# Performance work log

Hardware: AMD Instinct MI355X
Metric: run time of the kernel (lower is better)

Reference implementation:

```python
import jax, jax.numpy as jnp
import numpy as np

D_MODEL = 1024
NHEAD = 16
DK = D_MODEL // NHEAD  # 64
B, S = 2, 2048


def setup_inputs() -> dict:
    key = jax.random.key(0)
    ks = jax.random.split(key, 8)
    Q = jax.random.normal(ks[0], (B, S, D_MODEL), dtype=jnp.float32)
    K = jax.random.normal(ks[1], (B, S, D_MODEL), dtype=jnp.float32)
    V = jax.random.normal(ks[2], (B, S, D_MODEL), dtype=jnp.float32)
    additive_mask = jax.random.normal(ks[3], (S, S), dtype=jnp.float32)
    key_padding_mask = jnp.zeros((B, S), dtype=jnp.int32)  # ignored by the module
    # Per-head projection weights, stacked over heads: [H, d_model, dk]
    scale = 1.0 / np.sqrt(D_MODEL)
    WQ = jax.random.normal(ks[4], (NHEAD, D_MODEL, DK), dtype=jnp.float32) * scale
    WK = jax.random.normal(ks[5], (NHEAD, D_MODEL, DK), dtype=jnp.float32) * scale
    WV = jax.random.normal(ks[6], (NHEAD, D_MODEL, DK), dtype=jnp.float32) * scale
    WO = jax.random.normal(ks[7], (D_MODEL, D_MODEL), dtype=jnp.float32) * scale
    return {"Q": Q, "K": K, "V": V, "additive_mask": additive_mask,
            "key_padding_mask": key_padding_mask,
            "WQ": WQ, "WK": WK, "WV": WV, "WO": WO}


def reference(Q, K, V, additive_mask, key_padding_mask, WQ, WK, WV, WO):
    # Per-head projections, batched over heads: [B, H, S, dk]
    q = jnp.einsum('bsd,hdk->bhsk', Q, WQ)
    k = jnp.einsum('bsd,hdk->bhsk', K, WK)
    v = jnp.einsum('bsd,hdk->bhsk', V, WV)
    # scores: [B, H, S, S]; mask broadcasts over batch and head
    scores = jnp.einsum('bhqk,bhsk->bhqs', q, k) / np.sqrt(DK)
    scores = scores + additive_mask[None, None, :, :]
    attn = jax.nn.softmax(scores, axis=-1)
    o = jnp.einsum('bhqs,bhsk->bhqk', attn, v)  # [B, H, S, dk]
    # concat heads in head order == transpose + reshape to [B, S, H*dk]
    o = o.transpose(0, 2, 1, 3).reshape(Q.shape[0], Q.shape[1], D_MODEL)
    return o @ WO
```

## Files before the change

### kernel.cpp

```cpp
#include <hip/hip_runtime.h>
#include <hip/hip_bf16.h>
#include <stdint.h>

#define D_MODEL 1024
#define NHEAD 16
#define DKH 64
#define BATCH 2
#define SEQ 2048
#define LOG2E 1.44269504088896f

typedef __bf16 bf16_t;
typedef __bf16 bf16x8 __attribute__((ext_vector_type(8)));
typedef float f32x4 __attribute__((ext_vector_type(4)));
typedef float f32x16 __attribute__((ext_vector_type(16)));

__device__ __forceinline__ float fast_exp2(float x) {
#if __has_builtin(__builtin_amdgcn_exp2f)
  return __builtin_amdgcn_exp2f(x);
#else
  return exp2f(x);
#endif
}

__device__ __forceinline__ void gload_lds16(const bf16_t* g, bf16_t* l) {
  auto gp = (const __attribute__((address_space(1))) void*)(uintptr_t)g;
  auto lp = (__attribute__((address_space(3))) void*)(uintptr_t)l;
  __builtin_amdgcn_global_load_lds(gp, lp, 16, 0, 0);
}

__device__ __forceinline__ uint32_t pkbf(float lo, float hi) {
  bf16_t a = (bf16_t)lo, c = (bf16_t)hi;
  uint16_t ua, uc;
  __builtin_memcpy(&ua, &a, 2);
  __builtin_memcpy(&uc, &c, 2);
  return (uint32_t)ua | ((uint32_t)uc << 16);
}

__device__ __forceinline__ void perm32swap(uint32_t& a, uint32_t& b) {
  asm volatile("v_permlane32_swap_b32 %0, %1" : "+v"(a), "+v"(b));
}

__global__ void k_cvtw(const float* __restrict__ WQ, const float* __restrict__ WK,
                       const float* __restrict__ WV, const float* __restrict__ WO,
                       bf16_t* __restrict__ wt) {
  int j = blockIdx.x * 256 + threadIdx.x;
  int d = j & 1023, n = j >> 10;
  if (n < 3072) {
    int proj = n >> 10, h = (n >> 6) & 15, k = n & 63;
    const float* w = proj == 0 ? WQ : (proj == 1 ? WK : WV);
    float scale = proj == 0 ? (0.125f * LOG2E) : 1.0f;
    wt[j] = (bf16_t)(w[(h << 16) + (d << 6) + k] * scale);
  } else {
    wt[j] = (bf16_t)WO[(d << 10) + (n - 3072)];
  }
}

__global__ void k_maskg(const float* __restrict__ M, bf16_t* __restrict__ Mf) {
  int t = blockIdx.x * 256 + threadIdx.x;
  int wch = t & 7, lane = (t >> 3) & 63;
  int kvt = (t >> 9) & 31, qt = t >> 14;
  int h = lane >> 5, ql = lane & 31;
  int q = qt * 32 + ql;
  int t32 = wch >> 2, r2 = wch & 3;
  int kvb = kvt * 64 + t32 * 32 + 8 * r2 + 4 * h;
  float4 m4 = *reinterpret_cast<const float4*>(M + (size_t)q * SEQ + kvb);
  bf16_t o[4];
  o[0] = (bf16_t)(m4.x * LOG2E); o[1] = (bf16_t)(m4.y * LOG2E);
  o[2] = (bf16_t)(m4.z * LOG2E); o[3] = (bf16_t)(m4.w * LOG2E);
  *reinterpret_cast<ushort4*>(Mf + (size_t)t * 4) = *reinterpret_cast<ushort4*>(o);
}

__global__ __launch_bounds__(256)
void k_gemm_qkv(const float* __restrict__ Qs, const float* __restrict__ Ks32,
                const float* __restrict__ Vs32, const bf16_t* __restrict__ Bt,
                bf16_t* __restrict__ qh, bf16_t* __restrict__ Kf,
                bf16_t* __restrict__ Vf) {
  __shared__ __align__(16) bf16_t As[128 * 32];
  __shared__ __align__(16) bf16_t Bs[128 * 32];
  const int tid = threadIdx.x;
  const int lane = tid & 63, wave = tid >> 6;
  const int g = lane >> 4, lr = lane & 15;
  const int bm = blockIdx.x, bn = blockIdx.y;
  const int pn = bn >> 3;
  const float* Ap32 = pn == 0 ? Qs : (pn == 1 ? Ks32 : Vs32);
  const int wm = (wave >> 1) << 6, wn = (wave & 1) << 6;
  const int arow = tid >> 1, ako = (tid & 1) << 4;
  const float* aptr = Ap32 + (size_t)(bm * 128 + arow) * 1024 + ako;
  f32x4 acc[4][4] = {};

  float4 fA0 = *reinterpret_cast<const float4*>(aptr);
  float4 fA1 = *reinterpret_cast<const float4*>(aptr + 4);
  float4 fA2 = *reinterpret_cast<const float4*>(aptr + 8);
  float4 fA3 = *reinterpret_cast<const float4*>(aptr + 12);

  for (int kt = 0; kt < 1024; kt += 32) {
#pragma unroll
    for (int cc = 0; cc < 2; cc++) {
      int c = tid + cc * 256;
      int row = c >> 2, ko = (c & 3) << 3;
      gload_lds16(Bt + (size_t)(bn * 128 + row) * 1024 + kt + ko, Bs + c * 8);
    }
    {
      bf16x8 o0, o1;
      o0[0] = (bf16_t)fA0.x; o0[1] = (bf16_t)fA0.y; o0[2] = (bf16_t)fA0.z; o0[3] = (bf16_t)fA0.w;
      o0[4] = (bf16_t)fA1.x; o0[5] = (bf16_t)fA1.y; o0[6] = (bf16_t)fA1.z; o0[7] = (bf16_t)fA1.w;
      o1[0] = (bf16_t)fA2.x; o1[1] = (bf16_t)fA2.y; o1[2] = (bf16_t)fA2.z; o1[3] = (bf16_t)fA2.w;
      o1[4] = (bf16_t)fA3.x; o1[5] = (bf16_t)fA3.y; o1[6] = (bf16_t)fA3.z; o1[7] = (bf16_t)fA3.w;
      *reinterpret_cast<bf16x8*>(As + arow * 32 + ako) = o0;
      *reinterpret_cast<bf16x8*>(As + arow * 32 + ako + 8) = o1;
    }
    if (kt + 32 < 1024) {
      const float* np = aptr + kt + 32;
      fA0 = *reinterpret_cast<const float4*>(np);
      fA1 = *reinterpret_cast<const float4*>(np + 4);
      fA2 = *reinterpret_cast<const float4*>(np + 8);
      fA3 = *reinterpret_cast<const float4*>(np + 12);
    }
    __syncthreads();
    bf16x8 af[4], bfr[4];
#pragma unroll
    for (int t = 0; t < 4; t++)
      af[t] = *reinterpret_cast<const bf16x8*>(As + (wm + t * 16 + lr) * 32 + g * 8);
#pragma unroll
    for (int t = 0; t < 4; t++)
      bfr[t] = *reinterpret_cast<const bf16x8*>(Bs + (wn + t * 16 + lr) * 32 + g * 8);
    __builtin_amdgcn_s_setprio(1);
#pragma unroll
    for (int i = 0; i < 4; i++)
#pragma unroll
      for (int j = 0; j < 4; j++)
        acc[i][j] = __builtin_amdgcn_mfma_f32_16x16x32_bf16(af[i], bfr[j], acc[i][j], 0, 0, 0);
    __builtin_amdgcn_s_setprio(0);
    __syncthreads();
  }

#pragma unroll
  for (int i = 0; i < 4; i++)
#pragma unroll
    for (int j = 0; j < 4; j++)
#pragma unroll
      for (int e = 0; e < 4; e++) {
        int row = (bm << 7) + wm + i * 16 + g * 4 + e;
        int col = ((bn & 7) << 7) + wn + j * 16 + lr;
        float v = acc[i][j][e];
        int b = row >> 11, s = row & 2047, h = col >> 6, d = col & 63;
        size_t bh32 = (size_t)((b << 4) + h) * 32;
        if (pn == 0) {
          qh[((size_t)(((b << 4) + h) * SEQ + s) << 6) + d] = (bf16_t)v;
        } else if (pn == 1) {
          int kt2 = s >> 6, u = s & 63, t32 = u >> 5, ql2 = u & 31;
          int kk2 = d >> 4, hq2 = (d >> 3) & 1, e2 = d & 7;
          Kf[(bh32 + kt2) * 4096 + (t32 * 4 + kk2) * 512 + (hq2 * 32 + ql2) * 8 + e2] = (bf16_t)v;
        } else {
          int kt2 = s >> 6, u = s & 63, s2 = u >> 4, hq2 = (u >> 3) & 1, e2 = u & 7;
          int dkt = d >> 5, ql2 = d & 31;
          Vf[(bh32 + kt2) * 4096 + (dkt * 4 + s2) * 512 + (hq2 * 32 + ql2) * 8 + e2] = (bf16_t)v;
        }
      }
}

__global__ __launch_bounds__(256)
void k_gemm_wo(const bf16_t* __restrict__ A, const bf16_t* __restrict__ Bt,
               float* __restrict__ C) {
  __shared__ __align__(16) bf16_t As[64 * 32];
  __shared__ __align__(16) bf16_t Bs[128 * 32];
  const int tid = threadIdx.x;
  const int lane = tid & 63, wave = tid >> 6;
  const int g = lane >> 4, lr = lane & 15;
  const int bm = blockIdx.x, bn = blockIdx.y;
  const int wm = (wave >> 1) << 5, wn = (wave & 1) << 6;
  f32x4 acc[2][4] = {};

  for (int kt = 0; kt < 1024; kt += 32) {
    {
      int row = tid >> 2, ko = (tid & 3) << 3;
      gload_lds16(A + (size_t)(bm * 64 + row) * 1024 + kt + ko, As + tid * 8);
    }
#pragma unroll
    for (int cc = 0; cc < 2; cc++) {
      int c = tid + cc * 256;
      int row = c >> 2, ko = (c & 3) << 3;
      gload_lds16(Bt + (size_t)(bn * 128 + row) * 1024 + kt + ko, Bs + c * 8);
    }
    __syncthreads();
    bf16x8 af[2], bfr[4];
#pragma unroll
    for (int t = 0; t < 2; t++)
      af[t] = *reinterpret_cast<const bf16x8*>(As + (wm + t * 16 + lr) * 32 + g * 8);
#pragma unroll
    for (int t = 0; t < 4; t++)
      bfr[t] = *reinterpret_cast<const bf16x8*>(Bs + (wn + t * 16 + lr) * 32 + g * 8);
    __builtin_amdgcn_s_setprio(1);
#pragma unroll
    for (int i = 0; i < 2; i++)
#pragma unroll
      for (int j = 0; j < 4; j++)
        acc[i][j] = __builtin_amdgcn_mfma_f32_16x16x32_bf16(af[i], bfr[j], acc[i][j], 0, 0, 0);
    __builtin_amdgcn_s_setprio(0);
    __syncthreads();
  }
#pragma unroll
  for (int i = 0; i < 2; i++)
#pragma unroll
    for (int j = 0; j < 4; j++)
#pragma unroll
      for (int e = 0; e < 4; e++) {
        int row = (bm << 6) + wm + i * 16 + g * 4 + e;
        int col = (bn << 7) + wn + j * 16 + lr;
        C[(size_t)row * D_MODEL + col] = acc[i][j][e];
      }
}

__global__ __launch_bounds__(512, 4)
void k_attn6(const bf16_t* __restrict__ Qh, const bf16_t* __restrict__ Kf,
             const bf16_t* __restrict__ Vf, const bf16_t* __restrict__ Mf,
             bf16_t* __restrict__ O) {
  __shared__ __align__(16) bf16_t Ks[2][2][4096];
  __shared__ __align__(16) bf16_t Vs[2][2][4096];
  const int bid = blockIdx.x;
  const int xcd = bid & 7, loc = bid >> 3;
  const int bh = xcd * 4 + (loc >> 4);
  const int qtile = loc & 15;
  const int b = bh >> 4, h = bh & 15;
  const int tid = threadIdx.x, w = tid >> 6, lane = tid & 63;
  const int qw = w & 3, hh = w >> 2;
  const int hq = lane >> 5, ql = lane & 31;
  const int tid256 = tid & 255;
  const int qbase = qtile * 128 + qw * 32;
  const bf16_t* qp = Qh + (size_t)bh * SEQ * DKH;
  const bf16_t* kfp = Kf + (size_t)bh * 32 * 4096;
  const bf16_t* vfp = Vf + (size_t)bh * 32 * 4096;
  const int qt = qtile * 4 + qw;
  const bf16_t* mp = Mf + ((size_t)(qt * 32 + hh * 16) * 64 + lane) * 32;
  const int NIT = 16;

  bf16x8 aq[4];
#pragma unroll
  for (int kk = 0; kk < 4; kk++)
    aq[kk] = *reinterpret_cast<const bf16x8*>(
        qp + (size_t)(qbase + ql) * DKH + kk * 16 + hq * 8);

  f32x16 oacc[2] = {};
  float lsum = 0.f;

  auto stage = [&](int buf, int kt) {
#pragma unroll
    for (int cc = 0; cc < 2; cc++) {
      int c = tid256 + cc * 256;
      gload_lds16(kfp + (size_t)kt * 4096 + c * 8, &Ks[hh][buf][c * 8]);
      gload_lds16(vfp + (size_t)kt * 4096 + c * 8, &Vs[hh][buf][c * 8]);
    }
  };

  stage(0, hh * 16);
  bf16x8 mv[4];
#pragma unroll
  for (int j = 0; j < 4; j++)
    mv[j] = *reinterpret_cast<const bf16x8*>(mp + j * 8);
  __syncthreads();

  for (int it = 0; it < NIT; ++it) {
    const int cur = it & 1;
    if (it + 1 < NIT) stage(cur ^ 1, hh * 16 + it + 1);

    const bf16_t* kb = Ks[hh][cur];
    const bf16_t* vb = Vs[hh][cur];

    f32x16 p[2];
#pragma unroll
    for (int t32 = 0; t32 < 2; t32++) {
      f32x16 a = {};
      __builtin_amdgcn_s_setprio(1);
#pragma unroll
      for (int kk = 0; kk < 4; kk++) {
        bf16x8 bk = *reinterpret_cast<const bf16x8*>(kb + (t32 * 4 + kk) * 512 + lane * 8);
        a = __builtin_amdgcn_mfma_f32_32x32x16_bf16(bk, aq[kk], a, 0, 0, 0);
      }
      __builtin_amdgcn_s_setprio(0);
      p[t32] = a;
    }

    bf16x8 paf[4];
#pragma unroll
    for (int s = 0; s < 4; s++) {
      const int t32 = s >> 1, rb = (s & 1) * 8;
      float pes[8];
#pragma unroll
      for (int j = 0; j < 8; j++) {
        int v = t32 * 16 + rb + j;
        float x = p[t32][rb + j] + (float)mv[v >> 3][v & 7];
        float pe = fast_exp2(x);
        lsum += pe;
        pes[j] = pe;
      }
      uint32_t u0 = pkbf(pes[0], pes[1]), u1 = pkbf(pes[2], pes[3]);
      uint32_t w0 = pkbf(pes[4], pes[5]), w1 = pkbf(pes[6], pes[7]);
      perm32swap(u0, w0);
      perm32swap(u1, w1);
      union { uint32_t wd[4]; bf16x8 v8; } fu;
      fu.wd[0] = u0; fu.wd[1] = u1; fu.wd[2] = w0; fu.wd[3] = w1;
      paf[s] = fu.v8;
    }

    {
      const bf16_t* mn = mp + (size_t)((it + 1 < NIT) ? (it + 1) : it) * 2048;
#pragma unroll
      for (int j = 0; j < 4; j++)
        mv[j] = *reinterpret_cast<const bf16x8*>(mn + j * 8);
    }

#pragma unroll
    for (int dkt = 0; dkt < 2; dkt++) {
      __builtin_amdgcn_s_setprio(1);
#pragma unroll
      for (int s = 0; s < 4; s++) {
        bf16x8 bv = *reinterpret_cast<const bf16x8*>(vb + (dkt * 4 + s) * 512 + lane * 8);
        oacc[dkt] = __builtin_amdgcn_mfma_f32_32x32x16_bf16(paf[s], bv, oacc[dkt], 0, 0, 0);
      }
      __builtin_amdgcn_s_setprio(0);
    }
    __syncthreads();
  }

  float* smO = (float*)&Ks[0][0][0];
  float* smL = (float*)&Vs[0][0][0];
  if (w >= 4) {
    int base = (qw * 64 + lane) * 32;
#pragma unroll
    for (int dkt = 0; dkt < 2; dkt++)
#pragma unroll
      for (int cg = 0; cg < 4; cg++) {
        int chs = ((dkt * 4 + cg) ^ (lane & 7)) * 4;
        float4 val = {oacc[dkt][cg * 4], oacc[dkt][cg * 4 + 1],
                      oacc[dkt][cg * 4 + 2], oacc[dkt][cg * 4 + 3]};
        *reinterpret_cast<float4*>(&smO[base + chs]) = val;
      }
    smL[qw * 64 + lane] = lsum;
  }
  __syncthreads();
  if (w < 4) {
    int base = (qw * 64 + lane) * 32;
#pragma unroll
    for (int dkt = 0; dkt < 2; dkt++)
#pragma unroll
      for (int cg = 0; cg < 4; cg++) {
        int chs = ((dkt * 4 + cg) ^ (lane & 7)) * 4;
        float4 pv = *reinterpret_cast<const float4*>(&smO[base + chs]);
#pragma unroll
        for (int e = 0; e < 4; e++) oacc[dkt][cg * 4 + e] += pv[e];
      }
    lsum += smL[qw * 64 + lane];
    float lf = lsum + __shfl_xor(lsum, 32);
    float inv[16];
#pragma unroll
    for (int reg = 0; reg < 16; reg++) {
      int qrow = (reg & 3) + 8 * (reg >> 2) + 4 * hq;
      inv[reg] = 1.0f / __shfl(lf, qrow);
    }
#pragma unroll
    for (int dkt = 0; dkt < 2; dkt++)
#pragma unroll
      for (int reg = 0; reg < 16; reg++) {
        int qrow = (reg & 3) + 8 * (reg >> 2) + 4 * hq;
        float v = oacc[dkt][reg] * inv[reg];
        O[(size_t)(b * SEQ + qbase + qrow) * D_MODEL + (h << 6) + dkt * 32 + ql] = (bf16_t)v;
      }
  }
}

extern "C" void kernel_launch(void* const* d_in, const int* in_sizes, int n_in,
                              void* d_out, int out_size, void* d_ws, size_t ws_size,
                              hipStream_t stream) {
  const float* Q  = (const float*)d_in[0];
  const float* K  = (const float*)d_in[1];
  const float* V  = (const float*)d_in[2];
  const float* M  = (const float*)d_in[3];
  const float* WQ = (const float*)d_in[5];
  const float* WK = (const float*)d_in[6];
  const float* WV = (const float*)d_in[7];
  const float* WO = (const float*)d_in[8];

  char* ws = (char*)d_ws;
  const size_t MB = 1 << 20;
  bf16_t* Mf    = (bf16_t*)(ws + 24 * MB);
  bf16_t* WqkvT = (bf16_t*)(ws + 32 * MB);
  bf16_t* WoT   = (bf16_t*)(ws + 38 * MB);
  bf16_t* qh    = (bf16_t*)(ws + 40 * MB);
  bf16_t* Kf    = (bf16_t*)(ws + 48 * MB);
  bf16_t* Vf    = (bf16_t*)(ws + 56 * MB);
  bf16_t* Ob    = (bf16_t*)(ws + 64 * MB);

  k_maskg<<<4096, 256, 0, stream>>>(M, Mf);
  k_cvtw<<<16384, 256, 0, stream>>>(WQ, WK, WV, WO, WqkvT);

  k_gemm_qkv<<<dim3(32, 24), 256, 0, stream>>>(Q, K, V, WqkvT, qh, Kf, Vf);

  k_attn6<<<512, 512, 0, stream>>>(qh, Kf, Vf, Mf, Ob);

  k_gemm_wo<<<dim3(64, 8), 256, 0, stream>>>(Ob, WoT, (float*)d_out);
}
```

Before: 150.0 us.

## Read V fragments directly from global memory and drop V LDS staging

V tiles are no longer staged into shared memory. Each lane loads its V MFMA fragments straight from global memory, which are already laid out in fragment order. This shrinks the shared-memory footprint to 36 KB, and the launch-bounds hint is raised from 4 to 6 blocks per CU to allow more occupancy. The trade is that V loads are exposed global/L2 latency right before the PV MFMAs instead of being prefetched asynchronously, and the tighter register budget may spill.

```diff
diff --git a/kernel.cpp b/kernel.cpp
--- a/kernel.cpp
+++ b/kernel.cpp
@@ -211,12 +211,12 @@
       }
 }
 
-__global__ __launch_bounds__(512, 4)
-void k_attn6(const bf16_t* __restrict__ Qh, const bf16_t* __restrict__ Kf,
+__global__ __launch_bounds__(512, 6)
+void k_attn7(const bf16_t* __restrict__ Qh, const bf16_t* __restrict__ Kf,
              const bf16_t* __restrict__ Vf, const bf16_t* __restrict__ Mf,
              bf16_t* __restrict__ O) {
-  __shared__ __align__(16) bf16_t Ks[2][2][4096];
-  __shared__ __align__(16) bf16_t Vs[2][2][4096];
+  __shared__ __align__(16) char smem[36864];
+  bf16_t* KsB = reinterpret_cast<bf16_t*>(smem);
   const int bid = blockIdx.x;
   const int xcd = bid & 7, loc = bid >> 3;
   const int bh = xcd * 4 + (loc >> 4);
@@ -247,8 +247,8 @@
 #pragma unroll
     for (int cc = 0; cc < 2; cc++) {
       int c = tid256 + cc * 256;
-      gload_lds16(kfp + (size_t)kt * 4096 + c * 8, &Ks[hh][buf][c * 8]);
-      gload_lds16(vfp + (size_t)kt * 4096 + c * 8, &Vs[hh][buf][c * 8]);
+      gload_lds16(kfp + (size_t)kt * 4096 + c * 8,
+                  KsB + (hh * 2 + buf) * 4096 + c * 8);
     }
   };
 
@@ -263,8 +263,8 @@
     const int cur = it & 1;
     if (it + 1 < NIT) stage(cur ^ 1, hh * 16 + it + 1);
 
-    const bf16_t* kb = Ks[hh][cur];
-    const bf16_t* vb = Vs[hh][cur];
+    const bf16_t* kb = KsB + (hh * 2 + cur) * 4096;
+    const bf16_t* vt = vfp + (size_t)(hh * 16 + it) * 4096 + lane * 8;
 
     f32x16 p[2];
 #pragma unroll
@@ -311,19 +311,21 @@
 
 #pragma unroll
     for (int dkt = 0; dkt < 2; dkt++) {
+      bf16x8 bv[4];
+#pragma unroll
+      for (int s = 0; s < 4; s++)
+        bv[s] = *reinterpret_cast<const bf16x8*>(vt + (dkt * 4 + s) * 512);
       __builtin_amdgcn_s_setprio(1);
 #pragma unroll
-      for (int s = 0; s < 4; s++) {
-        bf16x8 bv = *reinterpret_cast<const bf16x8*>(vb + (dkt * 4 + s) * 512 + lane * 8);
-        oacc[dkt] = __builtin_amdgcn_mfma_f32_32x32x16_bf16(paf[s], bv, oacc[dkt], 0, 0, 0);
-      }
+      for (int s = 0; s < 4; s++)
+        oacc[dkt] = __builtin_amdgcn_mfma_f32_32x32x16_bf16(paf[s], bv[s], oacc[dkt], 0, 0, 0);
       __builtin_amdgcn_s_setprio(0);
     }
     __syncthreads();
   }
 
-  float* smO = (float*)&Ks[0][0][0];
-  float* smL = (float*)&Vs[0][0][0];
+  float* smO = (float*)smem;
+  float* smL = (float*)(smem + 32768);
   if (w >= 4) {
     int base = (qw * 64 + lane) * 32;
 #pragma unroll
@@ -395,7 +397,7 @@
 
   k_gemm_qkv<<<dim3(32, 24), 256, 0, stream>>>(Q, K, V, WqkvT, qh, Kf, Vf);
 
-  k_attn6<<<512, 512, 0, stream>>>(qh, Kf, Vf, Mf, Ob);
+  k_attn7<<<512, 512, 0, stream>>>(qh, Kf, Vf, Mf, Ob);
 
   k_gemm_wo<<<dim3(64, 8), 256, 0, stream>>>(Ob, WoT, (float*)d_out);
 }
```

Measured after the change: 298.2 us. 98.8% more time.
